# Performance work log

Measured on AMD Instinct MI355X. Metric: run time of the kernel, lower is better.

## Reference

```python
import jax, jax.numpy as jnp
import numpy as np

E = 8          # num_experts
K = 2          # top_k
R = 16         # lora_r
SCALING = 32.0 / 16.0  # lora_alpha / lora_r

B, S, H, I = 2, 2048, 2048, 8192


def setup_inputs() -> dict:
    key = jax.random.key(0)
    ks = jax.random.split(key, 11)
    inv_h = 1.0 / np.sqrt(H)
    inv_i = 1.0 / np.sqrt(I)
    return {
        "x": jax.random.normal(ks[0], (B, S, H), jnp.float32),
        "gate_W": jax.random.normal(ks[1], (I, H), jnp.float32) * inv_h,
        "up_W": jax.random.normal(ks[2], (I, H), jnp.float32) * inv_h,
        "down_W": jax.random.normal(ks[3], (H, I), jnp.float32) * inv_i,
        "router_W": jax.random.normal(ks[4], (E, H), jnp.float32) * 0.02,
        "gate_A": jax.random.normal(ks[5], (E, R, H), jnp.float32) * inv_h,
        "gate_B": jax.random.normal(ks[6], (E, I, R), jnp.float32) * 0.01,
        "up_A": jax.random.normal(ks[7], (E, R, H), jnp.float32) * inv_h,
        "up_B": jax.random.normal(ks[8], (E, I, R), jnp.float32) * 0.01,
        "down_A": jax.random.normal(ks[9], (E, R, I), jnp.float32) * inv_i,
        "down_B": jax.random.normal(ks[10], (E, H, R), jnp.float32) * 0.01,
    }


def _mixlora_forward(x, gate_W, up_W, down_W, router_W,
                     gate_A, gate_B, up_A, up_B, down_A, down_B):
    b, s, h = x.shape
    T = b * s
    xf = x.reshape(T, h)                                  # [T, H]

    # Shared base FFN projections (computed once for all experts)
    gate_out = xf @ gate_W.T                              # [T, I]
    up_out = xf @ up_W.T                                  # [T, I]

    # Router: softmax in fp32, top-k, renormalize selected weights
    logits = xf @ router_W.T                              # [T, E]
    probs = jax.nn.softmax(logits.astype(jnp.float32), axis=-1)
    w, idx = jax.lax.top_k(probs, K)                      # [T, K]
    w = w / jnp.sum(w, axis=-1, keepdims=True)

    # Dense per-(token, expert) combine weights; 0 for unselected experts
    onehot = jax.nn.one_hot(idx, E, dtype=probs.dtype)    # [T, K, E]
    w_dense = jnp.einsum('tke,tk->te', onehot, w)         # [T, E]

    # Load-balance aux loss: N * sum_i f_i * P_i
    f_i = jnp.sum(onehot, axis=(0, 1)) / T
    p_i = jnp.mean(probs, axis=0)
    aux_loss = E * jnp.dot(f_i, p_i)

    # Scan over experts, accumulating weighted intermediate and down-delta.
    # Since down_proj is linear, sum_k w_k * down(inter_k) = down(sum_k w_k * inter_k).
    def step(carry, p):
        acc_int, acc_dd = carry
        gA, gB, uA, uB, dA, dB, we = p                    # we: [T]
        gd = ((xf @ gA.T) @ gB.T) * SCALING               # [T, I]
        ud = ((xf @ uA.T) @ uB.T) * SCALING               # [T, I]
        inter = jax.nn.silu(gate_out + gd) * (up_out + ud)  # SwiGLU intermediate
        dd = ((inter @ dA.T) @ dB.T) * SCALING            # [T, H]
        we = we.astype(xf.dtype)[:, None]
        return (acc_int + we * inter, acc_dd + we * dd), None

    init = (jnp.zeros((T, gate_W.shape[0]), xf.dtype),
            jnp.zeros((T, h), xf.dtype))
    (acc_int, acc_dd), _ = jax.lax.scan(
        step, init, (gate_A, gate_B, up_A, up_B, down_A, down_B, w_dense.T))

    out = acc_int @ down_W.T + acc_dd                     # [T, H]
    return out.reshape(b, s, h), aux_loss


def reference(x, gate_W, up_W, down_W, router_W,
              gate_A, gate_B, up_A, up_B, down_A, down_B):
    return _mixlora_forward(x, gate_W, up_W, down_W, router_W,
                            gate_A, gate_B, up_A, up_B, down_A, down_B)
```

## Files before the change

### kernel.cpp

```cpp
#include <hip/hip_runtime.h>
#include <stdint.h>
#include <stddef.h>

#define DEVINL __device__ __forceinline__

typedef short sv8 __attribute__((ext_vector_type(8)));
typedef unsigned short usv8 __attribute__((ext_vector_type(8)));
typedef unsigned short usv4 __attribute__((ext_vector_type(4)));
typedef float f32x4 __attribute__((ext_vector_type(4)));

constexpr int T_TOK = 4096;
constexpr int H_DIM = 2048;
constexpr int I_DIM = 8192;
constexpr int E_NUM = 8;
constexpr int R_LORA = 16;
constexpr float SCALING = 2.0f;
constexpr int NQ = 4;
constexpr int TQ = T_TOK / NQ;
constexpr int PQ = TQ * 2;
constexpr int P_TOT = T_TOK * 2;

DEVINL float bf2f(unsigned short u) {
  union { uint32_t i; float f; } v; v.i = ((uint32_t)u) << 16; return v.f;
}
DEVINL unsigned short f2bf(float x) {
  union { float f; uint32_t i; } v; v.f = x;
  uint32_t r = v.i + 0x7FFFu + ((v.i >> 16) & 1u);
  return (unsigned short)(r >> 16);
}
DEVINL float bflo(uint32_t w) {
  union { uint32_t i; float f; } v; v.i = w << 16; return v.f;
}
DEVINL float bfhi(uint32_t w) {
  union { uint32_t i; float f; } v; v.i = w & 0xFFFF0000u; return v.f;
}

DEVINL f32x4 MFMA_BF16(sv8 a, sv8 b, f32x4 c) {
  return __builtin_amdgcn_mfma_f32_16x16x32_bf16(a, b, c, 0, 0, 0);
}

DEVINL void load16_to_lds(const void* g, void* l) {
  __builtin_amdgcn_global_load_lds(
      (const __attribute__((address_space(1))) uint32_t*)g,
      (__attribute__((address_space(3))) uint32_t*)l, 16, 0, 0);
}

#define BARRIER() __builtin_amdgcn_s_barrier()

__global__ void cast_f32_to_bf16(const float4* __restrict__ src, usv4* __restrict__ dst) {
  long i = (long)blockIdx.x * blockDim.x + threadIdx.x;
  float4 v = src[i];
  usv4 o;
  o[0] = f2bf(v.x); o[1] = f2bf(v.y); o[2] = f2bf(v.z); o[3] = f2bf(v.w);
  dst[i] = o;
}

__global__ void cast2_f32_to_bf16(const float4* __restrict__ src0, usv4* __restrict__ dst0,
                                  const float4* __restrict__ src1, usv4* __restrict__ dst1) {
  long i = (long)blockIdx.x * blockDim.x + threadIdx.x;
  const float4* s = blockIdx.y ? src1 : src0;
  usv4* d = blockIdx.y ? dst1 : dst0;
  float4 v = s[i];
  usv4 o;
  o[0] = f2bf(v.x); o[1] = f2bf(v.y); o[2] = f2bf(v.z); o[3] = f2bf(v.w);
  d[i] = o;
}

__global__ void zero_lcnt(int* lcnt) {
  if (threadIdx.x < E_NUM * NQ) lcnt[threadIdx.x] = 0;
}

__global__ void router_kernel(const float* __restrict__ x, const float* __restrict__ rW,
                              float* __restrict__ wbuf, int* __restrict__ idxb,
                              float* __restrict__ probs, int* __restrict__ lcnt,
                              int* __restrict__ lists, unsigned short* __restrict__ xf_bf) {
  const int wave = threadIdx.x >> 6, lane = threadIdx.x & 63;
  const int t = blockIdx.x * 4 + wave;
  const float* xr = x + (long)t * H_DIM;
  unsigned short* xbr = xf_bf + (long)t * H_DIM;
  float acc[E_NUM];
#pragma unroll
  for (int e = 0; e < E_NUM; ++e) acc[e] = 0.f;
  for (int h = lane; h < H_DIM; h += 64) {
    float xv = xr[h];
    xbr[h] = f2bf(xv);
#pragma unroll
    for (int e = 0; e < E_NUM; ++e) acc[e] += xv * rW[e * H_DIM + h];
  }
#pragma unroll
  for (int e = 0; e < E_NUM; ++e) {
#pragma unroll
    for (int off = 32; off; off >>= 1) acc[e] += __shfl_xor(acc[e], off);
  }
  if (lane == 0) {
    float mx = acc[0];
#pragma unroll
    for (int e = 1; e < E_NUM; ++e) mx = fmaxf(mx, acc[e]);
    float p[E_NUM];
    float s = 0.f;
#pragma unroll
    for (int e = 0; e < E_NUM; ++e) { p[e] = expf(acc[e] - mx); s += p[e]; }
    float inv = 1.f / s;
#pragma unroll
    for (int e = 0; e < E_NUM; ++e) p[e] *= inv;
    int e1 = 0;
    for (int e = 1; e < E_NUM; ++e) if (p[e] > p[e1]) e1 = e;
    int e2 = (e1 == 0) ? 1 : 0;
    for (int e = 0; e < E_NUM; ++e) if (e != e1 && p[e] > p[e2]) e2 = e;
    float w1 = p[e1], w2 = p[e2], wsum = w1 + w2;
    wbuf[t * 2 + 0] = w1 / wsum;
    wbuf[t * 2 + 1] = w2 / wsum;
    idxb[t * 2 + 0] = e1;
    idxb[t * 2 + 1] = e2;
#pragma unroll
    for (int e = 0; e < E_NUM; ++e) probs[(long)t * E_NUM + e] = p[e];
    const int q = t / TQ;
    int p1 = atomicAdd(&lcnt[e1 * NQ + q], 1); lists[(e1 * NQ + q) * TQ + p1] = t * 2 + 0;
    int p2 = atomicAdd(&lcnt[e2 * NQ + q], 1); lists[(e2 * NQ + q) * TQ + p2] = t * 2 + 1;
  }
}

__global__ void aux_kernel(const float* __restrict__ probs, const int* __restrict__ lcnt,
                           float* __restrict__ aux_out) {
  const int lane = threadIdx.x;
  float s[E_NUM];
#pragma unroll
  for (int e = 0; e < E_NUM; ++e) s[e] = 0.f;
  for (int t = lane; t < T_TOK; t += 64) {
#pragma unroll
    for (int e = 0; e < E_NUM; ++e) s[e] += probs[(long)t * E_NUM + e];
  }
#pragma unroll
  for (int e = 0; e < E_NUM; ++e) {
#pragma unroll
    for (int off = 32; off; off >>= 1) s[e] += __shfl_xor(s[e], off);
  }
  if (lane == 0) {
    float a = 0.f;
#pragma unroll
    for (int e = 0; e < E_NUM; ++e) {
      int cnt = 0;
#pragma unroll
      for (int q = 0; q < NQ; ++q) cnt += lcnt[e * NQ + q];
      a += ((float)cnt / (float)T_TOK) * (s[e] / (float)T_TOK);
    }
    *aux_out = (float)E_NUM * a;
  }
}

__global__ __launch_bounds__(256)
void lora_a_mfma_kernel(const unsigned short* __restrict__ xf_bf,
                        const unsigned short* __restrict__ gA_bf,
                        const unsigned short* __restrict__ uA_bf,
                        const int* __restrict__ lists, const int* __restrict__ lcnt,
                        float* __restrict__ vg, float* __restrict__ vu) {
  const int q = blockIdx.x / (E_NUM * 16);
  const int rem = blockIdx.x % (E_NUM * 16);
  const int e = rem >> 4;
  const int wave = threadIdx.x >> 6, lane = threadIdx.x & 63;
  const int grp = (rem & 15) * 4 + wave;
  const int npairs = lcnt[e * NQ + q];
  if (grp * 16 >= npairs) return;
  const int* lst = lists + (e * NQ + q) * TQ;
  const int slot = lane & 15;
  int pidx = grp * 16 + slot;
  int pair = lst[(pidx < npairs) ? pidx : grp * 16];
  int t = pair >> 1;
  const long kb = (long)blockIdx.y * 1024 + (lane >> 4) * 8;
  const unsigned short* arow = xf_bf + (long)t * H_DIM + kb;
  const unsigned short* bg = gA_bf + ((long)e * R_LORA + slot) * H_DIM + kb;
  const unsigned short* bu = uA_bf + ((long)e * R_LORA + slot) * H_DIM + kb;
  f32x4 ag = {}, au = {};
#pragma unroll 4
  for (int k = 0; k < 1024; k += 32) {
    sv8 a = *(const sv8*)(arow + k);
    ag = MFMA_BF16(a, *(const sv8*)(bg + k), ag);
    au = MFMA_BF16(a, *(const sv8*)(bu + k), au);
  }
  const int orow = (lane >> 4) * 4;
  const long base = (long)blockIdx.y * P_TOT;
#pragma unroll
  for (int rg = 0; rg < 4; ++rg) {
    int pidx2 = grp * 16 + orow + rg;
    if (pidx2 < npairs) {
      int pr = lst[pidx2];
      vg[(base + pr) * R_LORA + slot] = ag[rg];
      vu[(base + pr) * R_LORA + slot] = au[rg];
    }
  }
}

__global__ void reduce_uguu_kernel(const float* __restrict__ vg, const float* __restrict__ vu,
                                   float* __restrict__ ug, float* __restrict__ uu) {
  long i = (long)blockIdx.x * 256 + threadIdx.x;
  ug[i] = vg[i] + vg[(long)P_TOT * R_LORA + i];
  uu[i] = vu[i] + vu[(long)P_TOT * R_LORA + i];
}

template <bool F32OUT>
__global__ __launch_bounds__(512, 2)
void gemm8p_t(const unsigned short* __restrict__ A,
              const unsigned short* __restrict__ B0,
              const unsigned short* __restrict__ B1,
              unsigned short* __restrict__ Cb0,
              unsigned short* __restrict__ Cb1,
              float* __restrict__ Cf,
              int K, int lda, int ldb, int ldc,
              int az_off, int bz_off, long cz_off) {
  extern __shared__ unsigned short lds[];
  const int z = blockIdx.z;
  const unsigned short* __restrict__ Ap = A + (long)z * az_off;
  const unsigned short* __restrict__ Bp = (z ? B1 : B0) + (long)z * bz_off;
  const int tid = threadIdx.x;
  const int wave = tid >> 6, lane = tid & 63;
  const int wm = wave >> 2, wn = wave & 3;
  const long m0 = (long)blockIdx.y * 256;
  const long n0 = (long)blockIdx.x * 256;
  const int NT = K >> 6;

  const int lr = lane & 15;
  const int lc = (lane >> 4) * 8;
  const int xm = ((lane & 4) << 3) | ((lane & 2) << 3) | ((lane & 1) << 6);
  const int srow = tid >> 3;
  const int scol = (tid & 7) * 8;
  const int gcol = scol ^ (((tid >> 5) & 1) << 4) ^ (((tid >> 4) & 1) << 3)
                        ^ (((tid >> 3) & 1) << 5);

  f32x4 acc[8][4] = {};
  sv8 aF[4][2], bF[4][2];

  auto ldsAt = [&](int buf, int mat) -> unsigned short* {
    return lds + (((buf << 1) + mat) << 14);
  };
  auto stageA = [&](int buf, int R, long k0) {
    load16_to_lds(Ap + (m0 + R + srow) * (long)lda + k0 + gcol,
                  ldsAt(buf, 0) + ((R + srow) << 6) + scol);
  };
  auto stageB = [&](int buf, int R, long k0) {
    load16_to_lds(Bp + (n0 + R + srow) * (long)ldb + k0 + gcol,
                  ldsAt(buf, 1) + ((R + srow) << 6) + scol);
  };
  auto rdA = [&](int buf, int row16, int ks) -> sv8 {
    int bo = ((((row16 + lr) << 7) + ((ks * 32 + lc) << 1))) ^ xm;
    return *(const sv8*)((const char*)ldsAt(buf, 0) + bo);
  };
  auto rdB = [&](int buf, int row16, int ks) -> sv8 {
    int bo = ((((row16 + lr) << 7) + ((ks * 32 + lc) << 1))) ^ xm;
    return *(const sv8*)((const char*)ldsAt(buf, 1) + bo);
  };

  stageA(0, 0, 0); stageA(0, 64, 0); stageA(0, 128, 0); stageA(0, 192, 0);
  stageB(0, 0, 0); stageB(0, 64, 0); stageB(0, 128, 0); stageB(0, 192, 0);
  if (NT > 1) {
    stageA(1, 0, 64); stageA(1, 128, 64);
    asm volatile("s_waitcnt vmcnt(2)" ::: "memory");
  } else {
    asm volatile("s_waitcnt vmcnt(0)" ::: "memory");
  }
  BARRIER();

  for (int t = 0; t < NT; ++t) {
    const int P = t & 1, Q = P ^ 1;
    const long kQ = ((long)t + 1) << 6;
    const long kP2 = ((long)t + 2) << 6;
    const bool hQ = (t + 1) < NT, hP2 = (t + 2) < NT;

#pragma unroll
    for (int mf = 0; mf < 4; ++mf)
#pragma unroll
      for (int ks = 0; ks < 2; ++ks)
        aF[mf][ks] = rdA(P, wm * 128 + mf * 16, ks);
#pragma unroll
    for (int nf = 0; nf < 4; ++nf)
#pragma unroll
      for (int ks = 0; ks < 2; ++ks)
        bF[nf][ks] = rdB(P, wn * 64 + nf * 16, ks);
    if (hQ) {
      stageA(Q, 64, kQ); stageA(Q, 192, kQ);
      stageB(Q, 0, kQ); stageB(Q, 64, kQ); stageB(Q, 128, kQ); stageB(Q, 192, kQ);
    }
    __builtin_amdgcn_s_setprio(1);
#pragma unroll
    for (int mf = 0; mf < 4; ++mf)
#pragma unroll
      for (int nf = 0; nf < 4; ++nf)
#pragma unroll
        for (int ks = 0; ks < 2; ++ks)
          acc[mf][nf] = MFMA_BF16(aF[mf][ks], bF[nf][ks], acc[mf][nf]);
    __builtin_amdgcn_s_setprio(0);
    BARRIER();

#pragma unroll
    for (int mf = 0; mf < 4; ++mf)
#pragma unroll
      for (int ks = 0; ks < 2; ++ks)
        aF[mf][ks] = rdA(P, wm * 128 + 64 + mf * 16, ks);
    if (hP2) { stageA(P, 0, kP2); stageA(P, 128, kP2); }
    __builtin_amdgcn_s_setprio(1);
#pragma unroll
    for (int mf = 0; mf < 4; ++mf)
#pragma unroll
      for (int nf = 0; nf < 4; ++nf)
#pragma unroll
        for (int ks = 0; ks < 2; ++ks)
          acc[4 + mf][nf] = MFMA_BF16(aF[mf][ks], bF[nf][ks], acc[4 + mf][nf]);
    __builtin_amdgcn_s_setprio(0);
    if (hP2) {
      asm volatile("s_waitcnt vmcnt(2)" ::: "memory");
    } else {
      asm volatile("s_waitcnt vmcnt(0)" ::: "memory");
    }
    BARRIER();
  }

  const int rb = (lane >> 4) * 4, cb = lane & 15;
  if constexpr (F32OUT) {
    float* __restrict__ Cp = Cf + (long)z * cz_off;
#pragma unroll
    for (int mf = 0; mf < 8; ++mf)
#pragma unroll
      for (int nf = 0; nf < 4; ++nf) {
        long col = n0 + wn * 64 + nf * 16 + cb;
#pragma unroll
        for (int r = 0; r < 4; ++r) {
          long row = m0 + wm * 128 + mf * 16 + rb + r;
          Cp[row * ldc + col] = acc[mf][nf][r];
        }
      }
  } else {
    unsigned short* __restrict__ Cp = z ? Cb1 : Cb0;
#pragma unroll
    for (int mf = 0; mf < 8; ++mf)
#pragma unroll
      for (int nf = 0; nf < 4; ++nf) {
        long col = n0 + wn * 64 + nf * 16 + cb;
#pragma unroll
        for (int r = 0; r < 4; ++r) {
          long row = m0 + wm * 128 + mf * 16 + rb + r;
          Cp[row * ldc + col] = f2bf(acc[mf][nf][r]);
        }
      }
  }
}

__global__ __launch_bounds__(256)
void combine2_kernel(const unsigned short* __restrict__ g_bf,
                     const unsigned short* __restrict__ u_bf,
                     const unsigned short* __restrict__ gBp, const unsigned short* __restrict__ uBp,
                     const float* __restrict__ ug, const float* __restrict__ uu,
                     const float* __restrict__ wbuf,
                     const int* __restrict__ lists, const int* __restrict__ lcnt,
                     unsigned short* __restrict__ winter, int q0) {
  const int zq = blockIdx.z;
  const int q = q0 + zq;
  unsigned short* __restrict__ wint = winter + (size_t)zq * PQ * I_DIM;
  const int e = blockIdx.y >> 4, chunk = blockIdx.y & 15;
  const int npairs = lcnt[e * NQ + q];
  const int pbase = chunk * 64;
  if (pbase >= npairs) return;
  const int wave = threadIdx.x >> 6, lane = threadIdx.x & 63;
  const long i0 = (long)blockIdx.x * 256 + lane * 4;
  uint32_t gbp[32], ubp[32];
#pragma unroll
  for (int j = 0; j < 4; ++j) {
    const uint4* gp = (const uint4*)(gBp + ((long)e * I_DIM + i0 + j) * R_LORA);
    const uint4* up = (const uint4*)(uBp + ((long)e * I_DIM + i0 + j) * R_LORA);
    uint4 g0 = gp[0], g1 = gp[1], u0 = up[0], u1 = up[1];
    gbp[j * 8 + 0] = g0.x; gbp[j * 8 + 1] = g0.y; gbp[j * 8 + 2] = g0.z; gbp[j * 8 + 3] = g0.w;
    gbp[j * 8 + 4] = g1.x; gbp[j * 8 + 5] = g1.y; gbp[j * 8 + 6] = g1.z; gbp[j * 8 + 7] = g1.w;
    ubp[j * 8 + 0] = u0.x; ubp[j * 8 + 1] = u0.y; ubp[j * 8 + 2] = u0.z; ubp[j * 8 + 3] = u0.w;
    ubp[j * 8 + 4] = u1.x; ubp[j * 8 + 5] = u1.y; ubp[j * 8 + 6] = u1.z; ubp[j * 8 + 7] = u1.w;
  }
  for (int pl = 0; pl < 16; ++pl) {
    int pi = pbase + wave + pl * 4;
    if (pi >= npairs) break;
    int pair = lists[(e * NQ + q) * TQ + pi];
    int t = pair >> 1, plocal = pair - q * PQ;
    float w = wbuf[pair];
    const float2* ug2 = (const float2*)(ug + (long)pair * R_LORA);
    const float2* uu2 = (const float2*)(uu + (long)pair * R_LORA);
    usv4 gv = *(const usv4*)(g_bf + (long)t * I_DIM + i0);
    usv4 uv = *(const usv4*)(u_bf + (long)t * I_DIM + i0);
    float gd[4] = {0.f, 0.f, 0.f, 0.f}, ud[4] = {0.f, 0.f, 0.f, 0.f};
#pragma unroll
    for (int c = 0; c < 8; ++c) {
      float2 a = ug2[c], b = uu2[c];
#pragma unroll
      for (int j = 0; j < 4; ++j) {
        uint32_t gw = gbp[j * 8 + c], uw = ubp[j * 8 + c];
        gd[j] += a.x * bflo(gw) + a.y * bfhi(gw);
        ud[j] += b.x * bflo(uw) + b.y * bfhi(uw);
      }
    }
    usv4 o;
#pragma unroll
    for (int j = 0; j < 4; ++j) {
      float zg = bf2f(gv[j]) + SCALING * gd[j];
      float zu = bf2f(uv[j]) + SCALING * ud[j];
      float sil = zg / (1.f + __expf(-zg));
      o[j] = f2bf(w * sil * zu);
    }
    *(usv4*)(wint + (long)plocal * I_DIM + i0) = o;
  }
}

__global__ void acc_kernel(const unsigned short* __restrict__ winter,
                           unsigned short* __restrict__ acc_bf, int q0) {
  const int zq = blockIdx.z;
  const unsigned short* __restrict__ wint = winter + (size_t)zq * PQ * I_DIM;
  long gid = (long)blockIdx.x * 256 + threadIdx.x;
  int tl = (int)(gid >> 10);
  int ig = (int)(gid & 1023);
  int t = (q0 + zq) * TQ + tl;
  usv8 a = *(const usv8*)(wint + ((long)(tl * 2 + 0)) * I_DIM + ig * 8);
  usv8 b = *(const usv8*)(wint + ((long)(tl * 2 + 1)) * I_DIM + ig * 8);
  usv8 o;
#pragma unroll
  for (int j = 0; j < 8; ++j) o[j] = f2bf(bf2f(a[j]) + bf2f(b[j]));
  *(usv8*)(acc_bf + (long)t * I_DIM + ig * 8) = o;
}

__global__ __launch_bounds__(256)
void lorav_mfma_kernel(const unsigned short* __restrict__ winter,
                       const unsigned short* __restrict__ dA_bf,
                       const int* __restrict__ lists, const int* __restrict__ lcnt,
                       float* __restrict__ vv, int q0) {
  const int zq = blockIdx.z;
  const int q = q0 + zq;
  const unsigned short* __restrict__ wint = winter + (size_t)zq * PQ * I_DIM;
  const int e = blockIdx.x >> 4;
  const int wave = threadIdx.x >> 6, lane = threadIdx.x & 63;
  const int grp = (blockIdx.x & 15) * 4 + wave;
  const int npairs = lcnt[e * NQ + q];
  if (grp * 16 >= npairs) return;
  const int* lst = lists + (e * NQ + q) * TQ;
  const int slot = lane & 15;
  int pidx = grp * 16 + slot;
  int pair = lst[(pidx < npairs) ? pidx : grp * 16];
  int plocal = pair - q * PQ;
  const long kb = (long)blockIdx.y * 1024 + (lane >> 4) * 8;
  const unsigned short* arow = wint + (long)plocal * I_DIM + kb;
  const unsigned short* brow = dA_bf + ((long)e * R_LORA + slot) * I_DIM + kb;
  f32x4 acc = {};
#pragma unroll 4
  for (int k = 0; k < 1024; k += 32)
    acc = MFMA_BF16(*(const sv8*)(arow + k), *(const sv8*)(brow + k), acc);
  const int orow = (lane >> 4) * 4;
  const long base = (long)blockIdx.y * P_TOT;
#pragma unroll
  for (int rg = 0; rg < 4; ++rg) {
    int pidx2 = grp * 16 + orow + rg;
    if (pidx2 < npairs) {
      int pr = lst[pidx2];
      vv[(base + pr) * R_LORA + slot] = acc[rg];
    }
  }
}

__global__ void reduce_v_kernel(const float* __restrict__ vv, float* __restrict__ vbuf) {
  long i = (long)blockIdx.x * 256 + threadIdx.x;
  float s = 0.f;
#pragma unroll
  for (int kc = 0; kc < 8; ++kc) s += vv[(long)kc * P_TOT * R_LORA + i];
  vbuf[i] = s;
}

__global__ void ddmerge_kernel(const float* __restrict__ vbuf, const int* __restrict__ idxb,
                               const float* __restrict__ dB,
                               const float* __restrict__ p0, const float* __restrict__ p1,
                               float* __restrict__ out) {
  const int t = blockIdx.y;
  const int h = blockIdx.x * 256 + threadIdx.x;
  const int e0 = idxb[t * 2 + 0], e1 = idxb[t * 2 + 1];
  const float4* v0p = (const float4*)(vbuf + (long)(t * 2 + 0) * R_LORA);
  const float4* v1p = (const float4*)(vbuf + (long)(t * 2 + 1) * R_LORA);
  const float4* b0 = (const float4*)(dB + ((long)e0 * H_DIM + h) * R_LORA);
  const float4* b1 = (const float4*)(dB + ((long)e1 * H_DIM + h) * R_LORA);
  float dd = 0.f;
#pragma unroll
  for (int qq = 0; qq < 4; ++qq) {
    float4 v0 = v0p[qq], x0 = b0[qq];
    float4 v1 = v1p[qq], x1 = b1[qq];
    dd += v0.x * x0.x + v0.y * x0.y + v0.z * x0.z + v0.w * x0.w;
    dd += v1.x * x1.x + v1.y * x1.y + v1.z * x1.z + v1.w * x1.w;
  }
  long i = (long)t * H_DIM + h;
  out[i] = SCALING * dd + p0[i] + p1[i];
}

extern "C" void kernel_launch(void* const* d_in, const int* in_sizes, int n_in,
                              void* d_out, int out_size, void* d_ws, size_t ws_size,
                              hipStream_t stream) {
  (void)in_sizes; (void)n_in; (void)out_size;
  const float* x        = (const float*)d_in[0];
  const float* gate_W   = (const float*)d_in[1];
  const float* up_W     = (const float*)d_in[2];
  const float* down_W   = (const float*)d_in[3];
  const float* router_W = (const float*)d_in[4];
  const float* gate_A   = (const float*)d_in[5];
  const float* gate_B   = (const float*)d_in[6];
  const float* up_A     = (const float*)d_in[7];
  const float* up_B     = (const float*)d_in[8];
  const float* down_A   = (const float*)d_in[9];
  const float* down_B   = (const float*)d_in[10];
  float* out = (float*)d_out;

  char* ws = (char*)d_ws;
  size_t off = 0;
  auto take = [&](size_t bytes) -> char* {
    char* p = ws + off;
    off += (bytes + 255) & ~(size_t)255;
    return p;
  };
  unsigned short* xf_bf  = (unsigned short*)take((size_t)T_TOK * H_DIM * 2);
  unsigned short* gW_bf  = (unsigned short*)take((size_t)I_DIM * H_DIM * 2);
  unsigned short* uW_bf  = (unsigned short*)take((size_t)I_DIM * H_DIM * 2);
  unsigned short* dA_bf  = (unsigned short*)take((size_t)E_NUM * R_LORA * I_DIM * 2);
  unsigned short* g_bf   = (unsigned short*)take((size_t)T_TOK * I_DIM * 2);
  unsigned short* u_bf   = (unsigned short*)take((size_t)T_TOK * I_DIM * 2);
  float* wbuf  = (float*)take((size_t)P_TOT * 4);
  int*   idxb  = (int*)take((size_t)P_TOT * 4);
  float* ug    = (float*)take((size_t)P_TOT * R_LORA * 4);
  float* uu    = (float*)take((size_t)P_TOT * R_LORA * 4);
  float* vbuf  = (float*)take((size_t)P_TOT * R_LORA * 4);
  float* probs = (float*)take((size_t)T_TOK * E_NUM * 4);
  int*   lcnt  = (int*)take((size_t)E_NUM * NQ * 4);
  int*   lists = (int*)take((size_t)E_NUM * NQ * TQ * 4);
  const size_t qwin = (size_t)PQ * I_DIM * 2;
  size_t fixed = off;
  int QB = (ws_size >= fixed + 4 * qwin) ? 4 : 1;
  unsigned short* winterQ = (unsigned short*)take(qwin * QB);

  unsigned short* dW_bf  = gW_bf;
  unsigned short* acc_bf = g_bf;
  float* vg = (float*)winterQ;
  float* vu = (float*)(winterQ + (size_t)1 * 1024 * 1024 / 2);
  unsigned short* gA_bf = winterQ + (size_t)2 * 1024 * 1024 / 2;
  unsigned short* uA_bf = winterQ + (size_t)5 * 512 * 1024 / 2;
  float* vv = (float*)xf_bf;
  unsigned short* gB_bf = (unsigned short*)((char*)xf_bf + ((size_t)4 << 20));
  unsigned short* uB_bf = (unsigned short*)((char*)xf_bf + ((size_t)8 << 20));
  float* pbuf = (float*)u_bf;

  if (ws_size < off) return;

  zero_lcnt<<<1, 64, 0, stream>>>(lcnt);
  router_kernel<<<T_TOK / 4, 256, 0, stream>>>(x, router_W, wbuf, idxb, probs, lcnt, lists, xf_bf);
  aux_kernel<<<1, 64, 0, stream>>>(probs, lcnt, out + (size_t)T_TOK * H_DIM);

  cast2_f32_to_bf16<<<dim3((E_NUM * R_LORA * H_DIM / 4) / 256, 2), 256, 0, stream>>>(
      (const float4*)gate_A, (usv4*)gA_bf, (const float4*)up_A, (usv4*)uA_bf);
  lora_a_mfma_kernel<<<dim3(NQ * E_NUM * 16, 2), 256, 0, stream>>>(xf_bf, gA_bf, uA_bf, lists, lcnt, vg, vu);
  reduce_uguu_kernel<<<(P_TOT * R_LORA) / 256, 256, 0, stream>>>(vg, vu, ug, uu);

  cast2_f32_to_bf16<<<dim3((I_DIM * H_DIM / 4) / 256, 2), 256, 0, stream>>>(
      (const float4*)gate_W, (usv4*)gW_bf, (const float4*)up_W, (usv4*)uW_bf);
  cast_f32_to_bf16<<<(E_NUM * R_LORA * I_DIM / 4) / 256, 256, 0, stream>>>((const float4*)down_A, (usv4*)dA_bf);

  hipFuncSetAttribute(reinterpret_cast<const void*>(&gemm8p_t<false>),
                      hipFuncAttributeMaxDynamicSharedMemorySize, 131072);
  hipFuncSetAttribute(reinterpret_cast<const void*>(&gemm8p_t<true>),
                      hipFuncAttributeMaxDynamicSharedMemorySize, 131072);
  gemm8p_t<false><<<dim3(I_DIM / 256, T_TOK / 256, 2), 512, 131072, stream>>>(
      xf_bf, gW_bf, uW_bf, g_bf, u_bf, nullptr,
      H_DIM, H_DIM, H_DIM, I_DIM, 0, 0, 0);

  cast_f32_to_bf16<<<(H_DIM * I_DIM / 4) / 256, 256, 0, stream>>>((const float4*)down_W, (usv4*)dW_bf);
  cast2_f32_to_bf16<<<dim3((E_NUM * I_DIM * R_LORA / 4) / 256, 2), 256, 0, stream>>>(
      (const float4*)gate_B, (usv4*)gB_bf, (const float4*)up_B, (usv4*)uB_bf);

  for (int q0 = 0; q0 < NQ; q0 += QB) {
    combine2_kernel<<<dim3(I_DIM / 256, E_NUM * 16, QB), 256, 0, stream>>>(
        g_bf, u_bf, gB_bf, uB_bf, ug, uu, wbuf, lists, lcnt, winterQ, q0);
    acc_kernel<<<dim3((TQ * (I_DIM / 8)) / 256, 1, QB), 256, 0, stream>>>(winterQ, acc_bf, q0);
    lorav_mfma_kernel<<<dim3(E_NUM * 16, 8, QB), 256, 0, stream>>>(winterQ, dA_bf, lists, lcnt, vv, q0);
  }
  reduce_v_kernel<<<(P_TOT * R_LORA) / 256, 256, 0, stream>>>(vv, vbuf);

  gemm8p_t<true><<<dim3(H_DIM / 256, T_TOK / 256, 2), 512, 131072, stream>>>(
      acc_bf, dW_bf, dW_bf, nullptr, nullptr, pbuf,
      I_DIM / 2, I_DIM, I_DIM, H_DIM, I_DIM / 2, I_DIM / 2, (long)T_TOK * H_DIM);

  ddmerge_kernel<<<dim3(H_DIM / 256, T_TOK), 256, 0, stream>>>(
      vbuf, idxb, down_B, (const float*)pbuf,
      (const float*)(pbuf + (size_t)T_TOK * H_DIM), out);
}
```

Measured before the change: 1.039 ms.

## Replace split-K down GEMM with 256x128 tiles accumulating into output

The down-projection GEMM no longer splits K into two halves written to separate fp32 partial buffers and merged later. It now uses a 256x128 output tile over the full K, giving the same block count, and accumulates directly into the output that the LoRA dd kernel has already written. This removes the partial-buffer writes and reads and the merge pass, but each block now runs a K loop twice as long with a narrower B tile. The workspace check also gains a QB=2 option between 4 and 1.

```diff
diff --git a/kernel.cpp b/kernel.cpp
--- a/kernel.cpp
+++ b/kernel.cpp
@@ -197,7 +197,7 @@
   uu[i] = vu[i] + vu[(long)P_TOT * R_LORA + i];
 }
 
-template <bool F32OUT>
+template <bool F32OUT, int BN>
 __global__ __launch_bounds__(512, 2)
 void gemm8p_t(const unsigned short* __restrict__ A,
               const unsigned short* __restrict__ B0,
@@ -205,17 +205,18 @@
               unsigned short* __restrict__ Cb0,
               unsigned short* __restrict__ Cb1,
               float* __restrict__ Cf,
-              int K, int lda, int ldb, int ldc,
-              int az_off, int bz_off, long cz_off) {
+              int K, int lda, int ldb, int ldc) {
+  constexpr int NB = BN / 64;
+  constexpr int WN = BN / 4;
   extern __shared__ unsigned short lds[];
   const int z = blockIdx.z;
-  const unsigned short* __restrict__ Ap = A + (long)z * az_off;
-  const unsigned short* __restrict__ Bp = (z ? B1 : B0) + (long)z * bz_off;
+  const unsigned short* __restrict__ Ap = A;
+  const unsigned short* __restrict__ Bp = (z ? B1 : B0);
   const int tid = threadIdx.x;
   const int wave = tid >> 6, lane = tid & 63;
   const int wm = wave >> 2, wn = wave & 3;
   const long m0 = (long)blockIdx.y * 256;
-  const long n0 = (long)blockIdx.x * 256;
+  const long n0 = (long)blockIdx.x * BN;
   const int NT = K >> 6;
 
   const int lr = lane & 15;
@@ -226,31 +227,31 @@
   const int gcol = scol ^ (((tid >> 5) & 1) << 4) ^ (((tid >> 4) & 1) << 3)
                         ^ (((tid >> 3) & 1) << 5);
 
-  f32x4 acc[8][4] = {};
-  sv8 aF[4][2], bF[4][2];
-
-  auto ldsAt = [&](int buf, int mat) -> unsigned short* {
-    return lds + (((buf << 1) + mat) << 14);
-  };
+  f32x4 acc[8][NB] = {};
+  sv8 aF[4][2], bF[NB][2];
+
+  auto ldsA = [&](int buf) -> unsigned short* { return lds + buf * 16384; };
+  auto ldsB = [&](int buf) -> unsigned short* { return lds + 32768 + buf * (BN * 64); };
   auto stageA = [&](int buf, int R, long k0) {
     load16_to_lds(Ap + (m0 + R + srow) * (long)lda + k0 + gcol,
-                  ldsAt(buf, 0) + ((R + srow) << 6) + scol);
+                  ldsA(buf) + ((R + srow) << 6) + scol);
   };
   auto stageB = [&](int buf, int R, long k0) {
     load16_to_lds(Bp + (n0 + R + srow) * (long)ldb + k0 + gcol,
-                  ldsAt(buf, 1) + ((R + srow) << 6) + scol);
+                  ldsB(buf) + ((R + srow) << 6) + scol);
   };
   auto rdA = [&](int buf, int row16, int ks) -> sv8 {
     int bo = ((((row16 + lr) << 7) + ((ks * 32 + lc) << 1))) ^ xm;
-    return *(const sv8*)((const char*)ldsAt(buf, 0) + bo);
+    return *(const sv8*)((const char*)ldsA(buf) + bo);
   };
   auto rdB = [&](int buf, int row16, int ks) -> sv8 {
     int bo = ((((row16 + lr) << 7) + ((ks * 32 + lc) << 1))) ^ xm;
-    return *(const sv8*)((const char*)ldsAt(buf, 1) + bo);
+    return *(const sv8*)((const char*)ldsB(buf) + bo);
   };
 
   stageA(0, 0, 0); stageA(0, 64, 0); stageA(0, 128, 0); stageA(0, 192, 0);
-  stageB(0, 0, 0); stageB(0, 64, 0); stageB(0, 128, 0); stageB(0, 192, 0);
+#pragma unroll
+  for (int nb = 0; nb < NB; ++nb) stageB(0, nb * 64, 0);
   if (NT > 1) {
     stageA(1, 0, 64); stageA(1, 128, 64);
     asm volatile("s_waitcnt vmcnt(2)" ::: "memory");
@@ -271,19 +272,20 @@
       for (int ks = 0; ks < 2; ++ks)
         aF[mf][ks] = rdA(P, wm * 128 + mf * 16, ks);
 #pragma unroll
-    for (int nf = 0; nf < 4; ++nf)
+    for (int nf = 0; nf < NB; ++nf)
 #pragma unroll
       for (int ks = 0; ks < 2; ++ks)
-        bF[nf][ks] = rdB(P, wn * 64 + nf * 16, ks);
+        bF[nf][ks] = rdB(P, wn * WN + nf * 16, ks);
     if (hQ) {
       stageA(Q, 64, kQ); stageA(Q, 192, kQ);
-      stageB(Q, 0, kQ); stageB(Q, 64, kQ); stageB(Q, 128, kQ); stageB(Q, 192, kQ);
+#pragma unroll
+      for (int nb = 0; nb < NB; ++nb) stageB(Q, nb * 64, kQ);
     }
     __builtin_amdgcn_s_setprio(1);
 #pragma unroll
     for (int mf = 0; mf < 4; ++mf)
 #pragma unroll
-      for (int nf = 0; nf < 4; ++nf)
+      for (int nf = 0; nf < NB; ++nf)
 #pragma unroll
         for (int ks = 0; ks < 2; ++ks)
           acc[mf][nf] = MFMA_BF16(aF[mf][ks], bF[nf][ks], acc[mf][nf]);
@@ -300,7 +302,7 @@
 #pragma unroll
     for (int mf = 0; mf < 4; ++mf)
 #pragma unroll
-      for (int nf = 0; nf < 4; ++nf)
+      for (int nf = 0; nf < NB; ++nf)
 #pragma unroll
         for (int ks = 0; ks < 2; ++ks)
           acc[4 + mf][nf] = MFMA_BF16(aF[mf][ks], bF[nf][ks], acc[4 + mf][nf]);
@@ -315,16 +317,16 @@
 
   const int rb = (lane >> 4) * 4, cb = lane & 15;
   if constexpr (F32OUT) {
-    float* __restrict__ Cp = Cf + (long)z * cz_off;
+    float* __restrict__ Cp = Cf;
 #pragma unroll
     for (int mf = 0; mf < 8; ++mf)
 #pragma unroll
-      for (int nf = 0; nf < 4; ++nf) {
-        long col = n0 + wn * 64 + nf * 16 + cb;
+      for (int nf = 0; nf < NB; ++nf) {
+        long col = n0 + wn * WN + nf * 16 + cb;
 #pragma unroll
         for (int r = 0; r < 4; ++r) {
           long row = m0 + wm * 128 + mf * 16 + rb + r;
-          Cp[row * ldc + col] = acc[mf][nf][r];
+          Cp[row * ldc + col] += acc[mf][nf][r];
         }
       }
   } else {
@@ -332,8 +334,8 @@
 #pragma unroll
     for (int mf = 0; mf < 8; ++mf)
 #pragma unroll
-      for (int nf = 0; nf < 4; ++nf) {
-        long col = n0 + wn * 64 + nf * 16 + cb;
+      for (int nf = 0; nf < NB; ++nf) {
+        long col = n0 + wn * WN + nf * 16 + cb;
 #pragma unroll
         for (int r = 0; r < 4; ++r) {
           long row = m0 + wm * 128 + mf * 16 + rb + r;
@@ -465,10 +467,9 @@
   vbuf[i] = s;
 }
 
-__global__ void ddmerge_kernel(const float* __restrict__ vbuf, const int* __restrict__ idxb,
-                               const float* __restrict__ dB,
-                               const float* __restrict__ p0, const float* __restrict__ p1,
-                               float* __restrict__ out) {
+__global__ void dd_kernel(const float* __restrict__ vbuf, const int* __restrict__ idxb,
+                          const float* __restrict__ dB,
+                          float* __restrict__ out) {
   const int t = blockIdx.y;
   const int h = blockIdx.x * 256 + threadIdx.x;
   const int e0 = idxb[t * 2 + 0], e1 = idxb[t * 2 + 1];
@@ -484,8 +485,7 @@
     dd += v0.x * x0.x + v0.y * x0.y + v0.z * x0.z + v0.w * x0.w;
     dd += v1.x * x1.x + v1.y * x1.y + v1.z * x1.z + v1.w * x1.w;
   }
-  long i = (long)t * H_DIM + h;
-  out[i] = SCALING * dd + p0[i] + p1[i];
+  out[(long)t * H_DIM + h] = SCALING * dd;
 }
 
 extern "C" void kernel_launch(void* const* d_in, const int* in_sizes, int n_in,
@@ -528,7 +528,7 @@
   int*   lists = (int*)take((size_t)E_NUM * NQ * TQ * 4);
   const size_t qwin = (size_t)PQ * I_DIM * 2;
   size_t fixed = off;
-  int QB = (ws_size >= fixed + 4 * qwin) ? 4 : 1;
+  int QB = (ws_size >= fixed + 4 * qwin) ? 4 : (ws_size >= fixed + 2 * qwin) ? 2 : 1;
   unsigned short* winterQ = (unsigned short*)take(qwin * QB);
 
   unsigned short* dW_bf  = gW_bf;
@@ -540,7 +540,6 @@
   float* vv = (float*)xf_bf;
   unsigned short* gB_bf = (unsigned short*)((char*)xf_bf + ((size_t)4 << 20));
   unsigned short* uB_bf = (unsigned short*)((char*)xf_bf + ((size_t)8 << 20));
-  float* pbuf = (float*)u_bf;
 
   if (ws_size < off) return;
 
@@ -557,13 +556,12 @@
       (const float4*)gate_W, (usv4*)gW_bf, (const float4*)up_W, (usv4*)uW_bf);
   cast_f32_to_bf16<<<(E_NUM * R_LORA * I_DIM / 4) / 256, 256, 0, stream>>>((const float4*)down_A, (usv4*)dA_bf);
 
-  hipFuncSetAttribute(reinterpret_cast<const void*>(&gemm8p_t<false>),
+  hipFuncSetAttribute(reinterpret_cast<const void*>(&gemm8p_t<false, 256>),
                       hipFuncAttributeMaxDynamicSharedMemorySize, 131072);
-  hipFuncSetAttribute(reinterpret_cast<const void*>(&gemm8p_t<true>),
-                      hipFuncAttributeMaxDynamicSharedMemorySize, 131072);
-  gemm8p_t<false><<<dim3(I_DIM / 256, T_TOK / 256, 2), 512, 131072, stream>>>(
-      xf_bf, gW_bf, uW_bf, g_bf, u_bf, nullptr,
-      H_DIM, H_DIM, H_DIM, I_DIM, 0, 0, 0);
+  hipFuncSetAttribute(reinterpret_cast<const void*>(&gemm8p_t<true, 128>),
+                      hipFuncAttributeMaxDynamicSharedMemorySize, 98304);
+  gemm8p_t<false, 256><<<dim3(I_DIM / 256, T_TOK / 256, 2), 512, 131072, stream>>>(
+      xf_bf, gW_bf, uW_bf, g_bf, u_bf, nullptr, H_DIM, H_DIM, H_DIM, I_DIM);
 
   cast_f32_to_bf16<<<(H_DIM * I_DIM / 4) / 256, 256, 0, stream>>>((const float4*)down_W, (usv4*)dW_bf);
   cast2_f32_to_bf16<<<dim3((E_NUM * I_DIM * R_LORA / 4) / 256, 2), 256, 0, stream>>>(
@@ -577,11 +575,8 @@
   }
   reduce_v_kernel<<<(P_TOT * R_LORA) / 256, 256, 0, stream>>>(vv, vbuf);
 
-  gemm8p_t<true><<<dim3(H_DIM / 256, T_TOK / 256, 2), 512, 131072, stream>>>(
-      acc_bf, dW_bf, dW_bf, nullptr, nullptr, pbuf,
-      I_DIM / 2, I_DIM, I_DIM, H_DIM, I_DIM / 2, I_DIM / 2, (long)T_TOK * H_DIM);
-
-  ddmerge_kernel<<<dim3(H_DIM / 256, T_TOK), 256, 0, stream>>>(
-      vbuf, idxb, down_B, (const float*)pbuf,
-      (const float*)(pbuf + (size_t)T_TOK * H_DIM), out);
-}
+  dd_kernel<<<dim3(H_DIM / 256, T_TOK), 256, 0, stream>>>(vbuf, idxb, down_B, out);
+
+  gemm8p_t<true, 128><<<dim3(H_DIM / 128, T_TOK / 256, 1), 512, 98304, stream>>>(
+      acc_bf, dW_bf, nullptr, nullptr, nullptr, out, I_DIM, I_DIM, I_DIM, H_DIM);
+}
```

New measurement: 1.056 ms. No clear change (+1.6%).
